# Kernel tuning notes

Hardware: AMD Instinct MI355X
Metric: run time of the kernel (lower is better)

The kernel has to match this reference:

```python
import jax, jax.numpy as jnp
import numpy as np

B, C, T = 32, 512, 1024
SIG_LO, SIG_HI = 1.0, 10.0   # sigma_range
THR, BETA = 0.5, 0.95        # snn.Leaky(beta=0.95, threshold=thr)
KSIZE = 13


def setup_inputs() -> dict:
    key = jax.random.key(0)
    inp = jax.random.normal(key, (B, 1, C, T), dtype=jnp.float32)
    # nn.Parameter initialized to sigma_range.mean() = 5.5
    w = jnp.float32((SIG_LO + SIG_HI) / 2.0)
    return {"inp": inp, "w": w}


def _gaussian_kernel(sigma):
    # matches gaussian_kernel(size=13): linspace(-6, 6, 13), normalized
    r = jnp.linspace(-(KSIZE // 2), KSIZE // 2, KSIZE).astype(jnp.float32)
    k = jnp.exp(-0.5 * (r / sigma) ** 2)
    return k / k.sum()


def _atan_spike(u):
    # snntorch default ATan surrogate (alpha=2): fwd heaviside, bwd 1/(1+(pi*u)^2)
    soft = jnp.arctan(jnp.pi * u) / jnp.pi
    hard = (u > 0).astype(u.dtype)
    return soft + jax.lax.stop_gradient(hard - soft)


def reference(inp, w):
    x = inp[:, 0]  # (B, C, T)
    # w_eff = sigma_range.mean() + clamp(w, 1, 10); identical for every sample,
    # so the per-sample/per-timestep kernels of the original are all equal.
    sigma = (SIG_LO + SIG_HI) / 2.0 + jnp.clip(w, SIG_LO, SIG_HI)
    k = _gaussian_kernel(sigma)  # (13,)
    # 13-tap Gaussian smoothing along the channel axis, all timesteps at once
    x_mean = jax.lax.conv_general_dilated(
        x[:, None],                    # (B,1,C,T)
        k[None, None, :, None],        # (1,1,13,1)
        window_strides=(1, 1),
        padding=((KSIZE // 2, KSIZE // 2), (0, 0)),
        dimension_numbers=("NCHW", "OIHW", "NCHW"),
    )[:, 0]                            # (B,C,T)
    drive = jnp.transpose(x - x_mean, (2, 0, 1))  # (T,B,C)

    def step(mem, xt):
        # snntorch Leaky, reset_mechanism='subtract'; reset is detached
        reset = jax.lax.stop_gradient((mem > THR).astype(mem.dtype))
        mem = BETA * mem + xt - reset * THR
        spk = _atan_spike(mem - THR)
        return mem, spk

    mem0 = jnp.zeros((B, C), dtype=jnp.float32)
    _, spks = jax.lax.scan(step, mem0, drive)  # (T,B,C)
    return jnp.transpose(spks, (1, 2, 0))[:, None]  # (B,1,C,T)
```

## Files before the change

kernel.cpp:

```cpp
#include <hip/hip_runtime.h>
#include <math.h>

constexpr int Bn = 32;
constexpr int Cn = 512;
constexpr int Tn = 1024;
constexpr int KS = 13;

constexpr int CB   = 64;
constexpr int TT   = 64;
constexpr int NCH  = Tn / TT;
constexpr int DSTR = TT + 1;
constexpr int NB   = 2;
constexpr int NCW  = 4;
constexpr int SEG  = 16;
constexpr int HR   = SEG + KS - 1;


#define SCAN16(DV, TB)                                                   \
  _Pragma("unroll")                                                      \
  for (int j = 0; j < 16; ++j) {                                         \
    const float rthr = (mem > 0.5f) ? 0.5f : 0.0f;   \
    float a_  = __fmul_rn(0.95f, mem);                                   \
    float s2_ = __fadd_rn(a_, DV[j]);                                    \
    mem = __fsub_rn(s2_, rthr);                                          \
    const unsigned int bit = (mem > 0.5f) ? 1u : 0u;                     \
    if ((TB) + j < 32) lo |= bit << ((TB) + j);                          \
    else               hi |= bit << ((TB) + j - 32);                     \
  }

__global__ __launch_bounds__(384, 1)
void snn_fused(const float* __restrict__ x, const float* __restrict__ wp,
               float* __restrict__ out) {
  __shared__ float X0[NCW][HR][TT];
  __shared__ float X1[NCW][HR][TT];
  __shared__ float X2[NCW][HR][TT];
  __shared__ float D[NB][CB][DSTR];
  __shared__ unsigned long long Sb[NCH][CB];
  __shared__ unsigned int prod[NB];
  __shared__ unsigned int scanProg;

  const int tid = threadIdx.x;
  const int b   = blockIdx.y;
  const int c0  = blockIdx.x * CB;
  const long xbase = (long)b * Cn * Tn;

  if (tid < NB) prod[tid] = 0u;
  if (tid == NB) scanProg = 0u;

  float kw[KS];
  {
    float w  = wp[0];
    float wc = fminf(fmaxf(w, 1.0f), 10.0f);
    float sigma = __fadd_rn(5.5f, wc);
    float e[KS];
#pragma unroll
    for (int i = 0; i < KS; ++i) {
      float q = __fdiv_rn((float)(i - 6), sigma);
      float t = __fmul_rn(-0.5f, __fmul_rn(q, q));
      e[i] = (float)exp((double)t);
    }
    float s = __fadd_rn(
        __fadd_rn(__fadd_rn(e[0], e[1]), __fadd_rn(e[2], e[3])),
        __fadd_rn(__fadd_rn(e[4], e[5]), __fadd_rn(e[6], e[7])));
    s = __fadd_rn(s, e[8]);  s = __fadd_rn(s, e[9]);  s = __fadd_rn(s, e[10]);
    s = __fadd_rn(s, e[11]); s = __fadd_rn(s, e[12]);
#pragma unroll
    for (int i = 0; i < KS; ++i) kw[i] = __fdiv_rn(e[i], s);
  }

  __syncthreads();

  if (tid < 64) {
    const int c = tid;
    float mem = 0.0f;
    for (int k = 0; k < NCH; ++k) {
      const int slot = k & (NB - 1);
      const unsigned need = (unsigned)NCW * ((unsigned)(k >> 1) + 1u);
      while (__hip_atomic_load(&prod[slot], __ATOMIC_RELAXED,
                               __HIP_MEMORY_SCOPE_WORKGROUP) < need) {}
      __asm__ __volatile__("" ::: "memory");
      const float* Dc = &D[slot][c][0];
      unsigned int lo = 0u, hi = 0u;
      float dvA[16], dvB[16];
#pragma unroll
      for (int j = 0; j < 16; ++j) dvA[j] = Dc[j];
#pragma unroll
      for (int j = 0; j < 16; ++j) dvB[j] = Dc[16 + j];
      SCAN16(dvA, 0)
#pragma unroll
      for (int j = 0; j < 16; ++j) dvA[j] = Dc[32 + j];
      SCAN16(dvB, 16)
#pragma unroll
      for (int j = 0; j < 16; ++j) dvB[j] = Dc[48 + j];
      SCAN16(dvA, 32)
      SCAN16(dvB, 48)
      Sb[k][c] = ((unsigned long long)hi << 32) | (unsigned long long)lo;
      __asm__ __volatile__("s_waitcnt lgkmcnt(0)" ::: "memory");
      if (tid == 0)
        __hip_atomic_fetch_add(&scanProg, 1u, __ATOMIC_RELAXED,
                               __HIP_MEMORY_SCOPE_WORKGROUP);
    }
  } else if (tid < 64 + 64 * NCW) {
    const int ctid = tid - 64;
    const int col  = ctid & 63;
    const int w    = ctid >> 6;
    const int segS = w * SEG;
    const int cin0 = c0 + segS - 6;

    unsigned oobm = 0u;
#pragma unroll
    for (int j = 0; j < HR; ++j) {
      const int gc = cin0 + j;
      if (gc < 0 || gc >= Cn) oobm |= 1u << j;
    }
    const float* gp[7];
#pragma unroll
    for (int g = 0; g < 7; ++g) {
      int gc = cin0 + g * 4 + (col >> 4);
      gc = gc < 0 ? 0 : (gc > Cn - 1 ? Cn - 1 : gc);
      gp[g] = x + ((long)b * Cn + gc) * Tn + (col & 15) * 4;
    }

    auto dma = [&](int m, float (&Xs)[HR][TT]) {
#pragma unroll
      for (int g = 0; g < 7; ++g) {
        __builtin_amdgcn_global_load_lds(
            (const __attribute__((address_space(1))) void*)(gp[g] + m * TT),
            (__attribute__((address_space(3))) void*)(&Xs[g * 4][0]),
            16, 0, 0);
      }
    };
    auto convc = [&](float (&Xs)[HR][TT], int p) {
      float xs[HR];
#pragma unroll
      for (int j = 0; j < HR; ++j) {
        const float v = Xs[j][col];
        xs[j] = ((oobm >> j) & 1u) ? 0.0f : v;
      }
#pragma unroll
      for (int r = 0; r < SEG; ++r) {
        float acc = __fmul_rn(kw[0], xs[r]);
#pragma unroll
        for (int i = 1; i < KS; ++i)
          acc = __fadd_rn(acc, __fmul_rn(kw[i], xs[r + i]));
        D[p][segS + r][col] = __fsub_rn(xs[r + 6], acc);
      }
    };
    auto waitD = [&](int K) {
      if (K >= NB) {
        const unsigned need = (unsigned)(K - NB + 1);
        while (__hip_atomic_load(&scanProg, __ATOMIC_RELAXED,
                                 __HIP_MEMORY_SCOPE_WORKGROUP) < need) {}
        __asm__ __volatile__("" ::: "memory");
      }
    };
    auto signal = [&](int K) {
      __asm__ __volatile__("s_waitcnt lgkmcnt(0)" ::: "memory");
      if (col == 0)
        __hip_atomic_fetch_add(&prod[K & (NB - 1)], 1u, __ATOMIC_RELAXED,
                               __HIP_MEMORY_SCOPE_WORKGROUP);
    };

    dma(0, X0[w]);
    dma(1, X1[w]);
#define STEP(K, XC, XN)                                                  \
    do {                                                                 \
      if ((K) + 2 < NCH) dma((K) + 2, XN[w]);                            \
      waitD(K);                                                          \
      convc(XC[w], (K) & (NB - 1));                                      \
      signal(K);                                                         \
    } while (0)
    for (int kb = 0; kb < NCH - 1; kb += 3) {
      STEP(kb + 0, X0, X2);
      STEP(kb + 1, X1, X0);
      STEP(kb + 2, X2, X1);
    }
    STEP(NCH - 1, X0, X2);
#undef STEP
  } else {
    const int col = tid & 63;
    for (int k = 0; k < NCH; ++k) {
      while (__hip_atomic_load(&scanProg, __ATOMIC_RELAXED,
                               __HIP_MEMORY_SCOPE_WORKGROUP)
             < (unsigned)(k + 1)) {}
      __asm__ __volatile__("" ::: "memory");
      const int t0p = k * TT;
#pragma unroll 8
      for (int r = 0; r < CB; ++r) {
        const unsigned long long wb = Sb[k][r];
        const float v = ((wb >> col) & 1ull) ? 1.0f : 0.0f;
        out[xbase + (long)(c0 + r) * Tn + t0p + col] = v;
      }
    }
  }
}

extern "C" void kernel_launch(void* const* d_in, const int* in_sizes, int n_in,
                              void* d_out, int out_size, void* d_ws, size_t ws_size,
                              hipStream_t stream) {
  const float* x  = (const float*)d_in[0];
  const float* w  = (const float*)d_in[1];
  float* out      = (float*)d_out;
  dim3 grid(Cn / CB, Bn, 1);
  snn_fused<<<grid, 384, 0, stream>>>(x, w, out);
}
```

Baseline: 131.0 us.

## Add dedicated loader warp feeding shared halo tile to conv warps

Adds a seventh wavefront that issues all global-to-LDS async loads into a shared 76-row triple-buffered tile, instead of each conv wave loading its own overlapping 28-row halo. This removes the duplicated halo loads and moves load issue and vmcnt waits off the conv waves. Loader and conv waves now coordinate through per-chunk ready/consumed counters and an x-progress counter. The cost is one more wave per block and more spin-waiting on LDS atomics, and the correctness of the hand-set vmcnt counts depends on the exact number of loads in flight.

```diff
diff --git a/kernel.cpp b/kernel.cpp
--- a/kernel.cpp
+++ b/kernel.cpp
@@ -14,6 +14,9 @@
 constexpr int NCW  = 4;
 constexpr int SEG  = 16;
 constexpr int HR   = SEG + KS - 1;
+constexpr int XS   = 3;
+constexpr int XR   = CB + KS - 1;
+constexpr int ND   = XR / 4;
 
 
 #define SCAN16(DV, TB)                                                   \
@@ -28,15 +31,22 @@
     else               hi |= bit << ((TB) + j - 32);                     \
   }
 
-__global__ __launch_bounds__(384, 1)
+#define SPIN_GE(ADDR, VAL)                                               \
+  do {                                                                   \
+    while (__hip_atomic_load((ADDR), __ATOMIC_RELAXED,                   \
+                             __HIP_MEMORY_SCOPE_WORKGROUP) < (VAL)) {}   \
+    __asm__ __volatile__("" ::: "memory");                               \
+  } while (0)
+
+__global__ __launch_bounds__(448, 1)
 void snn_fused(const float* __restrict__ x, const float* __restrict__ wp,
                float* __restrict__ out) {
-  __shared__ float X0[NCW][HR][TT];
-  __shared__ float X1[NCW][HR][TT];
-  __shared__ float X2[NCW][HR][TT];
+  __shared__ float X[XS][XR][TT];
   __shared__ float D[NB][CB][DSTR];
   __shared__ unsigned long long Sb[NCH][CB];
-  __shared__ unsigned int prod[NB];
+  __shared__ unsigned int dReady[NCH];
+  __shared__ unsigned int consumed[NCH];
+  __shared__ unsigned int xprog;
   __shared__ unsigned int scanProg;
 
   const int tid = threadIdx.x;
@@ -44,8 +54,9 @@
   const int c0  = blockIdx.x * CB;
   const long xbase = (long)b * Cn * Tn;
 
-  if (tid < NB) prod[tid] = 0u;
-  if (tid == NB) scanProg = 0u;
+  if (tid < NCH) { dReady[tid] = 0u; consumed[tid] = 0u; }
+  if (tid == NCH)     xprog = 0u;
+  if (tid == NCH + 1) scanProg = 0u;
 
   float kw[KS];
   {
@@ -70,16 +81,15 @@
 
   __syncthreads();
 
-  if (tid < 64) {
-    const int c = tid;
+  const int w    = tid >> 6;
+  const int lane = tid & 63;
+
+  if (w == 0) {
+    const int c = lane;
     float mem = 0.0f;
     for (int k = 0; k < NCH; ++k) {
-      const int slot = k & (NB - 1);
-      const unsigned need = (unsigned)NCW * ((unsigned)(k >> 1) + 1u);
-      while (__hip_atomic_load(&prod[slot], __ATOMIC_RELAXED,
-                               __HIP_MEMORY_SCOPE_WORKGROUP) < need) {}
-      __asm__ __volatile__("" ::: "memory");
-      const float* Dc = &D[slot][c][0];
+      SPIN_GE(&dReady[k], (unsigned)NCW);
+      const float* Dc = &D[k & (NB - 1)][c][0];
       unsigned int lo = 0u, hi = 0u;
       float dvA[16], dvB[16];
 #pragma unroll
@@ -96,94 +106,53 @@
       SCAN16(dvB, 48)
       Sb[k][c] = ((unsigned long long)hi << 32) | (unsigned long long)lo;
       __asm__ __volatile__("s_waitcnt lgkmcnt(0)" ::: "memory");
-      if (tid == 0)
+      if (lane == 0)
         __hip_atomic_fetch_add(&scanProg, 1u, __ATOMIC_RELAXED,
                                __HIP_MEMORY_SCOPE_WORKGROUP);
     }
-  } else if (tid < 64 + 64 * NCW) {
-    const int ctid = tid - 64;
-    const int col  = ctid & 63;
-    const int w    = ctid >> 6;
-    const int segS = w * SEG;
-    const int cin0 = c0 + segS - 6;
+  } else if (w <= NCW) {
+    const int g    = w - 1;
+    const int segS = g * SEG;
+    const int col  = lane;
 
     unsigned oobm = 0u;
 #pragma unroll
     for (int j = 0; j < HR; ++j) {
-      const int gc = cin0 + j;
+      const int gc = c0 + segS - 6 + j;
       if (gc < 0 || gc >= Cn) oobm |= 1u << j;
     }
-    const float* gp[7];
-#pragma unroll
-    for (int g = 0; g < 7; ++g) {
-      int gc = cin0 + g * 4 + (col >> 4);
-      gc = gc < 0 ? 0 : (gc > Cn - 1 ? Cn - 1 : gc);
-      gp[g] = x + ((long)b * Cn + gc) * Tn + (col & 15) * 4;
-    }
-
-    auto dma = [&](int m, float (&Xs)[HR][TT]) {
-#pragma unroll
-      for (int g = 0; g < 7; ++g) {
-        __builtin_amdgcn_global_load_lds(
-            (const __attribute__((address_space(1))) void*)(gp[g] + m * TT),
-            (__attribute__((address_space(3))) void*)(&Xs[g * 4][0]),
-            16, 0, 0);
-      }
-    };
-    auto convc = [&](float (&Xs)[HR][TT], int p) {
+
+    for (int k = 0; k < NCH; ++k) {
+      SPIN_GE(&xprog, (unsigned)(k + 1));
+      const float* Xs = &X[k % XS][segS][0];
       float xs[HR];
 #pragma unroll
       for (int j = 0; j < HR; ++j) {
-        const float v = Xs[j][col];
+        const float v = Xs[j * TT + col];
         xs[j] = ((oobm >> j) & 1u) ? 0.0f : v;
       }
+      if (k >= NB) SPIN_GE(&scanProg, (unsigned)(k - NB + 1));
+      float (*Dp)[DSTR] = D[k & (NB - 1)];
 #pragma unroll
       for (int r = 0; r < SEG; ++r) {
         float acc = __fmul_rn(kw[0], xs[r]);
 #pragma unroll
         for (int i = 1; i < KS; ++i)
           acc = __fadd_rn(acc, __fmul_rn(kw[i], xs[r + i]));
-        D[p][segS + r][col] = __fsub_rn(xs[r + 6], acc);
-      }
-    };
-    auto waitD = [&](int K) {
-      if (K >= NB) {
-        const unsigned need = (unsigned)(K - NB + 1);
-        while (__hip_atomic_load(&scanProg, __ATOMIC_RELAXED,
-                                 __HIP_MEMORY_SCOPE_WORKGROUP) < need) {}
-        __asm__ __volatile__("" ::: "memory");
-      }
-    };
-    auto signal = [&](int K) {
+        Dp[segS + r][col] = __fsub_rn(xs[r + 6], acc);
+      }
       __asm__ __volatile__("s_waitcnt lgkmcnt(0)" ::: "memory");
-      if (col == 0)
-        __hip_atomic_fetch_add(&prod[K & (NB - 1)], 1u, __ATOMIC_RELAXED,
-                               __HIP_MEMORY_SCOPE_WORKGROUP);
-    };
-
-    dma(0, X0[w]);
-    dma(1, X1[w]);
-#define STEP(K, XC, XN)                                                  \
-    do {                                                                 \
-      if ((K) + 2 < NCH) dma((K) + 2, XN[w]);                            \
-      waitD(K);                                                          \
-      convc(XC[w], (K) & (NB - 1));                                      \
-      signal(K);                                                         \
-    } while (0)
-    for (int kb = 0; kb < NCH - 1; kb += 3) {
-      STEP(kb + 0, X0, X2);
-      STEP(kb + 1, X1, X0);
-      STEP(kb + 2, X2, X1);
-    }
-    STEP(NCH - 1, X0, X2);
-#undef STEP
-  } else {
-    const int col = tid & 63;
-    for (int k = 0; k < NCH; ++k) {
-      while (__hip_atomic_load(&scanProg, __ATOMIC_RELAXED,
-                               __HIP_MEMORY_SCOPE_WORKGROUP)
-             < (unsigned)(k + 1)) {}
-      __asm__ __volatile__("" ::: "memory");
+      if (col == 0) {
+        __hip_atomic_fetch_add(&dReady[k], 1u, __ATOMIC_RELAXED,
+                               __HIP_MEMORY_SCOPE_WORKGROUP);
+        __hip_atomic_fetch_add(&consumed[k], 1u, __ATOMIC_RELAXED,
+                               __HIP_MEMORY_SCOPE_WORKGROUP);
+      }
+    }
+  } else if (w == NCW + 1) {
+    const int col = lane;
+    for (int k = 0; k < NCH; ++k) {
+      SPIN_GE(&scanProg, (unsigned)(k + 1));
       const int t0p = k * TT;
 #pragma unroll 8
       for (int r = 0; r < CB; ++r) {
@@ -191,6 +160,41 @@
         const float v = ((wb >> col) & 1ull) ? 1.0f : 0.0f;
         out[xbase + (long)(c0 + r) * Tn + t0p + col] = v;
       }
+    }
+  } else {
+    const float* gpd[ND];
+#pragma unroll
+    for (int d = 0; d < ND; ++d) {
+      int gc = c0 - 6 + d * 4 + (lane >> 4);
+      gc = gc < 0 ? 0 : (gc > Cn - 1 ? Cn - 1 : gc);
+      gpd[d] = x + ((long)b * Cn + gc) * Tn + (lane & 15) * 4;
+    }
+    auto issue = [&](int m) {
+      const int slot = m % XS;
+#pragma unroll
+      for (int d = 0; d < ND; ++d) {
+        __builtin_amdgcn_global_load_lds(
+            (const __attribute__((address_space(1))) void*)(gpd[d] + m * TT),
+            (__attribute__((address_space(3))) void*)(&X[slot][d * 4][0]),
+            16, 0, 0);
+      }
+    };
+
+    issue(0);
+    issue(1);
+    for (int k = 0; k < NCH; ++k) {
+      if (k + 2 < NCH) {
+        if (k >= 1) SPIN_GE(&consumed[k - 1], (unsigned)NCW);
+        issue(k + 2);
+        __asm__ __volatile__("s_waitcnt vmcnt(38)" ::: "memory");
+      } else if (k == NCH - 2) {
+        __asm__ __volatile__("s_waitcnt vmcnt(19)" ::: "memory");
+      } else {
+        __asm__ __volatile__("s_waitcnt vmcnt(0)" ::: "memory");
+      }
+      if (lane == 0)
+        __hip_atomic_fetch_add(&xprog, 1u, __ATOMIC_RELAXED,
+                               __HIP_MEMORY_SCOPE_WORKGROUP);
     }
   }
 }
@@ -202,5 +206,5 @@
   const float* w  = (const float*)d_in[1];
   float* out      = (float*)d_out;
   dim3 grid(Cn / CB, Bn, 1);
-  snn_fused<<<grid, 384, 0, stream>>>(x, w, out);
+  snn_fused<<<grid, 448, 0, stream>>>(x, w, out);
 }
```

Result: no change. 128.8 us (-1.7%).
